# Kernel optimization log

Hardware: AMD Instinct MI355X
Metric: run time of the kernel (lower is better)

The kernel has to match this reference:

```python
import jax, jax.numpy as jnp
import numpy as np

ROPE_BASE = 10000.0

def _rope_cos_sin(T, d, dtype):
    inv_freq = 1.0 / (ROPE_BASE ** (jnp.arange(0, d, 2, dtype=jnp.float32) / d))
    t = jnp.arange(T, dtype=jnp.float32)
    freqs = t[:, None] * inv_freq[None, :]           # [T, d/2]
    emb = jnp.concatenate([freqs, freqs], axis=-1)   # [T, d]
    return jnp.cos(emb).astype(dtype), jnp.sin(emb).astype(dtype)

def _rotate_half(x):
    x1, x2 = jnp.split(x, 2, axis=-1)
    return jnp.concatenate([-x2, x1], axis=-1)

def setup_inputs() -> dict:
    key = jax.random.key(0)
    k1, k2, k3, k4 = jax.random.split(key, 4)
    B, T, C, H = 4, 4096, 1024, 64
    x = jax.random.normal(k1, (B, T, C), dtype=jnp.float32)
    s = 1.0 / np.sqrt(C)
    Wq = jax.random.normal(k2, (H, C), dtype=jnp.float32) * s
    Wk = jax.random.normal(k3, (H, C), dtype=jnp.float32) * s
    Wv = jax.random.normal(k4, (H, C), dtype=jnp.float32) * s
    return {"x": x, "Wq": Wq, "Wk": Wk, "Wv": Wv}

def reference(x, Wq, Wk, Wv):
    B, T, C = x.shape
    H = Wq.shape[0]
    q = jnp.einsum('btc,hc->bth', x, Wq)
    k = jnp.einsum('btc,hc->bth', x, Wk)
    v = jnp.einsum('btc,hc->bth', x, Wv)
    cos, sin = _rope_cos_sin(T, H, x.dtype)
    q = q * cos + _rotate_half(q) * sin
    k = k * cos + _rotate_half(k) * sin
    # NOTE: original scales by dim_model**-0.5 (C), not head_size
    wei = jnp.einsum('bth,bsh->bts', q, k) * (C ** -0.5)
    causal = jnp.tril(jnp.ones((T, T), dtype=bool))
    wei = jnp.where(causal, wei, -jnp.inf)
    wei = jax.nn.softmax(wei, axis=-1)
    # dropout p=0.0 (identity)
    out = jnp.einsum('bts,bsh->bth', wei, v)
    return out
```

## Files before the change

### kernel.cpp

```cpp
#include <hip/hip_runtime.h>
#include <hip/hip_bf16.h>
#include <math.h>

typedef __attribute__((ext_vector_type(8))) __bf16 bf16x8;
typedef __attribute__((ext_vector_type(4))) float f32x4;
typedef __attribute__((ext_vector_type(16))) float f32x16;
typedef __attribute__((ext_vector_type(4))) float float4_t;
typedef __attribute__((ext_vector_type(4))) unsigned int uint4_t;

#define NB 4
#define TSEQ 4096
#define CD 1024
#define HD 64
#define NCH 16
#define CHT 4
#define QBL 16

static __device__ __forceinline__ unsigned short f2bf(float f) {
    union { float f; unsigned u; } v; v.f = f;
    unsigned r = v.u + 0x7fffu + ((v.u >> 16) & 1u);
    return (unsigned short)(r >> 16);
}
static __device__ __forceinline__ float bf2f(unsigned short u) {
    union { unsigned int i; float f; } v; v.i = ((unsigned int)u) << 16;
    return v.f;
}
static __device__ __forceinline__ unsigned int pk2(float a, float b) {
    union { __bf16 h[2]; unsigned int u; } x;
    x.h[0] = (__bf16)a; x.h[1] = (__bf16)b;
    return x.u;
}

__global__ __launch_bounds__(256) void wcvt_kernel(const float* __restrict__ wq,
                                                   const float* __restrict__ wk,
                                                   const float* __restrict__ wv,
                                                   unsigned short* __restrict__ wb) {
    int i = blockIdx.x * 256 + threadIdx.x;
    int j = i >> 10;
    int col = i & 1023;
    int jb = j >> 4, off = j & 15;
    int sub = ((jb & 1) << 5) | ((jb & 2) << 3);
    int srcrow = (jb < 8) ? (sub + off) : ((jb - 8) * 16 + off);
    const float* src = (jb < 4) ? wq : ((jb < 8) ? wk : wv);
    wb[i] = f2bf(src[srcrow * 1024 + col]);
}

__global__ __launch_bounds__(256) void qkv_kernel(const float* __restrict__ x,
                                                  const unsigned short* __restrict__ wb,
                                                  unsigned short* __restrict__ qo,
                                                  unsigned short* __restrict__ ko,
                                                  unsigned short* __restrict__ vt) {
    __shared__ unsigned short xs[64][72];
    __shared__ unsigned short ws[96][72];
    const int tid = threadIdx.x;
    const int wave = tid >> 6, lane = tid & 63;
    const int lr = lane & 15;
    const int lk = (lane >> 4) << 3;
    const int rowg = (lane >> 4) << 2;
    const int row0 = blockIdx.x * 64;
    const int phase = blockIdx.y;

    f32x4 acc[6];
#pragma unroll
    for (int i = 0; i < 6; ++i) acc[i] = (f32x4){0.f, 0.f, 0.f, 0.f};

    const int sr = tid >> 2;
    const int sc = (tid & 3) << 4;
    const unsigned short* wbp = wb + (size_t)(96 * phase) * CD;

    for (int k0 = 0; k0 < CD; k0 += 64) {
        __syncthreads();
        {
            const float4_t* s4 =
                reinterpret_cast<const float4_t*>(x + (size_t)(row0 + sr) * CD + k0 + sc);
            float4_t f0 = s4[0], f1 = s4[1], f2 = s4[2], f3 = s4[3];
            uint4_t w0, w1;
            w0[0] = pk2(f0[0], f0[1]); w0[1] = pk2(f0[2], f0[3]);
            w0[2] = pk2(f1[0], f1[1]); w0[3] = pk2(f1[2], f1[3]);
            w1[0] = pk2(f2[0], f2[1]); w1[1] = pk2(f2[2], f2[3]);
            w1[2] = pk2(f3[0], f3[1]); w1[3] = pk2(f3[2], f3[3]);
            *reinterpret_cast<uint4_t*>(&xs[sr][sc]) = w0;
            *reinterpret_cast<uint4_t*>(&xs[sr][sc + 8]) = w1;
        }
#pragma unroll
        for (int i = 0; i < 3; ++i) {
            int u = tid + (i << 8);
            int r = u >> 3, c = (u & 7) << 3;
            *reinterpret_cast<uint4_t*>(&ws[r][c]) =
                *reinterpret_cast<const uint4_t*>(wbp + (size_t)r * CD + k0 + c);
        }
        __syncthreads();
#pragma unroll
        for (int kk = 0; kk < 2; ++kk) {
            bf16x8 a = *reinterpret_cast<const bf16x8*>(&xs[wave * 16 + lr][kk * 32 + lk]);
#pragma unroll
            for (int c = 0; c < 6; ++c) {
                bf16x8 bfr = *reinterpret_cast<const bf16x8*>(&ws[c * 16 + lr][kk * 32 + lk]);
                acc[c] = __builtin_amdgcn_mfma_f32_16x16x32_bf16(a, bfr, acc[c], 0, 0, 0);
            }
        }
    }

    const int gr0 = row0 + wave * 16 + rowg;
    const int bidx = gr0 >> 12;
    const int tb = gr0 & (TSEQ - 1);
    const float sc2 = 0.045084218764560315f;
    const float l2b = 0.4152410118609215f;
    const float invf0 = exp2f(-(float)lr * l2b);
    const float invf1 = exp2f(-(float)(lr + 16) * l2b);
#pragma unroll
    for (int r = 0; r < 4; ++r) {
        float t = (float)(tb + r);
        float s0, c0, s1, c1;
        sincosf(t * invf0, &s0, &c0);
        sincosf(t * invf1, &s1, &c1);
        size_t ro = (size_t)(gr0 + r) * HD;
        if (phase == 0) {
            float lo, hi;
            lo = acc[0][r]; hi = acc[1][r];
            qo[ro + 0 + lr]  = f2bf((lo * c0 - hi * s0) * sc2);
            qo[ro + 32 + lr] = f2bf((hi * c0 + lo * s0) * sc2);
            lo = acc[2][r]; hi = acc[3][r];
            qo[ro + 16 + lr] = f2bf((lo * c1 - hi * s1) * sc2);
            qo[ro + 48 + lr] = f2bf((hi * c1 + lo * s1) * sc2);
            lo = acc[4][r]; hi = acc[5][r];
            ko[ro + 0 + lr]  = f2bf(lo * c0 - hi * s0);
            ko[ro + 32 + lr] = f2bf(hi * c0 + lo * s0);
        } else {
            float lo = acc[0][r], hi = acc[1][r];
            ko[ro + 16 + lr] = f2bf(lo * c1 - hi * s1);
            ko[ro + 48 + lr] = f2bf(hi * c1 + lo * s1);
            size_t vbase = (size_t)bidx * HD * TSEQ + (size_t)(tb + r);
            vt[vbase + (size_t)(0 + lr) * TSEQ]  = f2bf(acc[2][r]);
            vt[vbase + (size_t)(16 + lr) * TSEQ] = f2bf(acc[3][r]);
            vt[vbase + (size_t)(32 + lr) * TSEQ] = f2bf(acc[4][r]);
            vt[vbase + (size_t)(48 + lr) * TSEQ] = f2bf(acc[5][r]);
        }
    }
}

__global__ __launch_bounds__(512, 4) void attn_partial(const unsigned short* __restrict__ q,
                                                       const unsigned short* __restrict__ k,
                                                       const unsigned short* __restrict__ vt,
                                                       unsigned short* __restrict__ po,
                                                       float* __restrict__ pm,
                                                       float* __restrict__ pl) {
    const int chunk = blockIdx.x, qb = blockIdx.y, b = blockIdx.z;
    const int ktend_blk = 4 * qb + 3;
    const int kt0 = chunk * CHT;
    if (kt0 > ktend_blk) return;
    const int ktend = min(ktend_blk, kt0 + CHT - 1);

    __shared__ unsigned short ks[64][72];
    __shared__ unsigned short vs[64][72];
    const int tid = threadIdx.x;
    const int wave = tid >> 6, lane = tid & 63;
    const int l31 = lane & 31;
    const int h = lane >> 5;
    const int h8 = h << 3;
    const int qrow0 = qb * 256 + wave * 32;
    const int qpos = qrow0 + l31;

    const unsigned short* qb_ = q + ((size_t)(b * TSEQ + qpos)) * HD + h8;
    bf16x8 qf[4];
#pragma unroll
    for (int s = 0; s < 4; ++s)
        qf[s] = *reinterpret_cast<const bf16x8*>(qb_ + 16 * s);

    f32x16 oacc[2];
#pragma unroll
    for (int dt = 0; dt < 2; ++dt)
#pragma unroll
        for (int r = 0; r < 16; ++r) oacc[dt][r] = 0.f;
    float mreg = -1.0e30f;
    float lsum = 0.f;

    const int srow = tid >> 3;
    const int scol = (tid & 7) << 3;
    const unsigned short* kbase = k + (size_t)b * TSEQ * HD;
    const unsigned short* vbase = vt + (size_t)b * HD * TSEQ;
    uint4_t kr, vr;

    auto loadtile = [&](int kt) {
        const int s0l = kt * 64;
        kr = *reinterpret_cast<const uint4_t*>(kbase + (size_t)(s0l + srow) * HD + scol);
        vr = *reinterpret_cast<const uint4_t*>(vbase + (size_t)srow * TSEQ + s0l + scol);
    };

    loadtile(kt0);

    for (int kt = kt0; kt <= ktend; ++kt) {
        const int s0 = kt * 64;
        __syncthreads();
        *reinterpret_cast<uint4_t*>(&ks[srow][scol]) = kr;
        *reinterpret_cast<uint4_t*>(&vs[srow][scol]) = vr;
        __syncthreads();
        if (kt < ktend) loadtile(kt + 1);

        if (s0 > qrow0 + 31) continue;

        f32x16 sacc[2];
#pragma unroll
        for (int blk = 0; blk < 2; ++blk)
#pragma unroll
            for (int r = 0; r < 16; ++r) sacc[blk][r] = 0.f;
        __builtin_amdgcn_s_setprio(1);
#pragma unroll
        for (int s = 0; s < 4; ++s) {
            bf16x8 ka = *reinterpret_cast<const bf16x8*>(&ks[l31][16 * s + h8]);
            bf16x8 kb2 = *reinterpret_cast<const bf16x8*>(&ks[32 + l31][16 * s + h8]);
            sacc[0] = __builtin_amdgcn_mfma_f32_32x32x16_bf16(ka, qf[s], sacc[0], 0, 0, 0);
            sacc[1] = __builtin_amdgcn_mfma_f32_32x32x16_bf16(kb2, qf[s], sacc[1], 0, 0, 0);
        }
        __builtin_amdgcn_s_setprio(0);

        if (s0 + 63 > qrow0) {
#pragma unroll
            for (int blk = 0; blk < 2; ++blk)
#pragma unroll
                for (int r = 0; r < 16; ++r) {
                    int kvpos = s0 + 32 * blk + (r & 3) + ((r >> 2) << 3) + (h << 2);
                    if (kvpos > qpos) sacc[blk][r] = -INFINITY;
                }
        }

        float tm[8];
#pragma unroll
        for (int r = 0; r < 8; ++r)
            tm[r] = fmaxf(fmaxf(sacc[0][r], sacc[0][r + 8]),
                          fmaxf(sacc[1][r], sacc[1][r + 8]));
#pragma unroll
        for (int r = 0; r < 4; ++r) tm[r] = fmaxf(tm[r], tm[r + 4]);
        float mx = fmaxf(fmaxf(tm[0], tm[1]), fmaxf(tm[2], tm[3]));
        mx = fmaxf(mx, __shfl_xor(mx, 32, 64));

        const bool newmax = !__all(mx <= mreg + 7.0f);
        if (newmax) {
            float mnew = fmaxf(mreg, mx);
            float corr = __builtin_amdgcn_exp2f(mreg - mnew);
            mreg = mnew;
            lsum *= corr;
#pragma unroll
            for (int dt = 0; dt < 2; ++dt)
#pragma unroll
                for (int r = 0; r < 16; ++r) oacc[dt][r] *= corr;
        }

        float pvv[2][16];
#pragma unroll
        for (int blk = 0; blk < 2; ++blk)
#pragma unroll
            for (int r = 0; r < 16; ++r)
                pvv[blk][r] = __builtin_amdgcn_exp2f(sacc[blk][r] - mreg);
        float ts[8];
#pragma unroll
        for (int r = 0; r < 8; ++r)
            ts[r] = (pvv[0][r] + pvv[0][r + 8]) + (pvv[1][r] + pvv[1][r + 8]);
#pragma unroll
        for (int r = 0; r < 4; ++r) ts[r] += ts[r + 4];
        float psum = (ts[0] + ts[1]) + (ts[2] + ts[3]);
        psum += __shfl_xor(psum, 32, 64);
        lsum += psum;

        unsigned int cw[2][4][2];
#pragma unroll
        for (int blk = 0; blk < 2; ++blk)
#pragma unroll
            for (int G = 0; G < 4; ++G) {
                cw[blk][G][0] = pk2(pvv[blk][4 * G], pvv[blk][4 * G + 1]);
                cw[blk][G][1] = pk2(pvv[blk][4 * G + 2], pvv[blk][4 * G + 3]);
            }

        const bool hif = (h == 1);
        __builtin_amdgcn_s_setprio(1);
#pragma unroll
        for (int s = 0; s < 4; ++s) {
            const int blk = s >> 1, base = (s & 1) << 1;
            unsigned int a0 = cw[blk][base][0],     a1 = cw[blk][base][1];
            unsigned int b0 = cw[blk][base + 1][0], b1 = cw[blk][base + 1][1];
            unsigned int s0w = hif ? a0 : b0;
            unsigned int s1w = hif ? a1 : b1;
            unsigned int r0 = __shfl_xor(s0w, 32, 64);
            unsigned int r1 = __shfl_xor(s1w, 32, 64);
            uint4_t pw;
            pw[0] = hif ? r0 : a0;
            pw[1] = hif ? r1 : a1;
            pw[2] = hif ? b0 : r0;
            pw[3] = hif ? b1 : r1;
            bf16x8 pfrag = *reinterpret_cast<const bf16x8*>(&pw);
            bf16x8 v0 = *reinterpret_cast<const bf16x8*>(&vs[l31][16 * s + h8]);
            bf16x8 v1 = *reinterpret_cast<const bf16x8*>(&vs[32 + l31][16 * s + h8]);
            oacc[0] = __builtin_amdgcn_mfma_f32_32x32x16_bf16(v0, pfrag, oacc[0], 0, 0, 0);
            oacc[1] = __builtin_amdgcn_mfma_f32_32x32x16_bf16(v1, pfrag, oacc[1], 0, 0, 0);
        }
        __builtin_amdgcn_s_setprio(0);
    }

    const int slot = (((b << 4) + qb) << 4) + chunk;
    unsigned short* pob = po + (size_t)slot * 16384;
#pragma unroll
    for (int dt = 0; dt < 2; ++dt)
#pragma unroll
        for (int r = 0; r < 16; ++r) {
            int d = 32 * dt + (r & 3) + ((r >> 2) << 3) + (h << 2);
            pob[d * 256 + wave * 32 + l31] = f2bf(oacc[dt][r]);
        }
    if (h == 0) {
        pm[slot * 256 + wave * 32 + l31] = mreg;
        pl[slot * 256 + wave * 32 + l31] = lsum;
    }
}

__global__ __launch_bounds__(256) void attn_combine(const unsigned short* __restrict__ po,
                                                    const float* __restrict__ pm,
                                                    const float* __restrict__ pl,
                                                    float* __restrict__ out) {
    __shared__ float sm[64][17];
    const int bq = blockIdx.x;
    const int dg = blockIdx.y;
    const int qt = bq & 63;
    const int b = bq >> 6;
    const int qb = qt >> 2, quarter = qt & 3;
    const int nch = qb + 1;
    const int qi = threadIdx.x & 63;
    const int jj = threadIdx.x >> 6;
    const int slotb = (((b << 4) + qb) << 4);
    const int qoff = quarter * 64 + qi;

    float pmv[NCH];
#pragma unroll
    for (int c = 0; c < NCH; ++c)
        pmv[c] = (c < nch) ? pm[(size_t)(slotb + c) * 256 + qoff] : -1.0e30f;
    float tmv[NCH];
#pragma unroll
    for (int c = 0; c < NCH; ++c) tmv[c] = pmv[c];
#pragma unroll
    for (int s = NCH / 2; s >= 1; s >>= 1)
#pragma unroll
        for (int c = 0; c < NCH / 2; ++c)
            if (c < s) tmv[c] = fmaxf(tmv[c], tmv[c + s]);
    const float M = tmv[0];

    float L = 0.f;
    float a0 = 0.f, a1 = 0.f, a2 = 0.f, a3 = 0.f;
    const int dbase = dg * 16 + jj * 4;
#pragma unroll 4
    for (int c = 0; c < nch; ++c) {
        float w = exp2f(pmv[c] - M);
        L += w * pl[(size_t)(slotb + c) * 256 + qoff];
        const unsigned short* p = po + (size_t)(slotb + c) * 16384 + dbase * 256 + qoff;
        a0 += w * bf2f(p[0]);
        a1 += w * bf2f(p[256]);
        a2 += w * bf2f(p[512]);
        a3 += w * bf2f(p[768]);
    }
    const float inv = 1.f / L;
    sm[qi][jj * 4 + 0] = a0 * inv;
    sm[qi][jj * 4 + 1] = a1 * inv;
    sm[qi][jj * 4 + 2] = a2 * inv;
    sm[qi][jj * 4 + 3] = a3 * inv;
    __syncthreads();
    const int row = threadIdx.x >> 2;
    const int c4 = (threadIdx.x & 3) << 2;
    float4_t f;
#pragma unroll
    for (int e = 0; e < 4; ++e) f[e] = sm[row][c4 + e];
    *reinterpret_cast<float4_t*>(out + (size_t)bq * 4096 + row * 64 + dg * 16 + c4) = f;
}

extern "C" void kernel_launch(void* const* d_in, const int* in_sizes, int n_in,
                              void* d_out, int out_size, void* d_ws, size_t ws_size,
                              hipStream_t stream) {
    const float* x = (const float*)d_in[0];
    const float* wq = (const float*)d_in[1];
    const float* wk = (const float*)d_in[2];
    const float* wv = (const float*)d_in[3];
    float* out = (float*)d_out;

    unsigned short* wb = (unsigned short*)d_ws;
    unsigned short* qb = wb + 3 * HD * CD;
    unsigned short* kb = qb + (size_t)NB * TSEQ * HD;
    unsigned short* vtb = kb + (size_t)NB * TSEQ * HD;
    unsigned short* pob = vtb + (size_t)NB * TSEQ * HD;
    float* pm = (float*)(pob + (size_t)1024 * 16384);
    float* pl = pm + (size_t)1024 * 256;

    wcvt_kernel<<<768, 256, 0, stream>>>(wq, wk, wv, wb);
    qkv_kernel<<<dim3(256, 2), 256, 0, stream>>>(x, wb, qb, kb, vtb);
    attn_partial<<<dim3(NCH, QBL, NB), 512, 0, stream>>>(qb, kb, vtb, pob, pm, pl);
    attn_combine<<<dim3(NB * 64, 4), 256, 0, stream>>>(pob, pm, pl, out);
}
```

Before: 66.64 us.

## Retile QKV projection to read x once and halve attention split-K chunks

The QKV projection now loads each 32-row tile of x once and computes all 192 output columns in one block, with waves split across rows and column halves. Before, two phase blocks each re-read and re-converted the same 64 rows of x. The attention split-K factor drops from 16 chunks of 4 key tiles to 8 chunks of 8, which halves the partial-output storage and the combine traffic. The trade-off is longer serial work per attention block and fewer blocks, which can hurt load balance on the causal triangle.

```diff
diff --git a/kernel.cpp b/kernel.cpp
--- a/kernel.cpp
+++ b/kernel.cpp
@@ -12,8 +12,8 @@
 #define TSEQ 4096
 #define CD 1024
 #define HD 64
-#define NCH 16
-#define CHT 4
+#define NCH 8
+#define CHT 8
 #define QBL 16
 
 static __device__ __forceinline__ unsigned short f2bf(float f) {
@@ -50,58 +50,55 @@
                                                   unsigned short* __restrict__ qo,
                                                   unsigned short* __restrict__ ko,
                                                   unsigned short* __restrict__ vt) {
-    __shared__ unsigned short xs[64][72];
-    __shared__ unsigned short ws[96][72];
+    __shared__ unsigned short xs[32][72];
+    __shared__ unsigned short ws[192][72];
     const int tid = threadIdx.x;
     const int wave = tid >> 6, lane = tid & 63;
     const int lr = lane & 15;
     const int lk = (lane >> 4) << 3;
     const int rowg = (lane >> 4) << 2;
-    const int row0 = blockIdx.x * 64;
-    const int phase = blockIdx.y;
+    const int wr = wave & 1, wc = wave >> 1;
+    const int row0 = blockIdx.x * 32;
 
     f32x4 acc[6];
 #pragma unroll
     for (int i = 0; i < 6; ++i) acc[i] = (f32x4){0.f, 0.f, 0.f, 0.f};
 
-    const int sr = tid >> 2;
-    const int sc = (tid & 3) << 4;
-    const unsigned short* wbp = wb + (size_t)(96 * phase) * CD;
+    const int xr = tid >> 3;
+    const int xc = (tid & 7) << 3;
 
     for (int k0 = 0; k0 < CD; k0 += 64) {
         __syncthreads();
         {
             const float4_t* s4 =
-                reinterpret_cast<const float4_t*>(x + (size_t)(row0 + sr) * CD + k0 + sc);
-            float4_t f0 = s4[0], f1 = s4[1], f2 = s4[2], f3 = s4[3];
-            uint4_t w0, w1;
+                reinterpret_cast<const float4_t*>(x + (size_t)(row0 + xr) * CD + k0 + xc);
+            float4_t f0 = s4[0], f1 = s4[1];
+            uint4_t w0;
             w0[0] = pk2(f0[0], f0[1]); w0[1] = pk2(f0[2], f0[3]);
             w0[2] = pk2(f1[0], f1[1]); w0[3] = pk2(f1[2], f1[3]);
-            w1[0] = pk2(f2[0], f2[1]); w1[1] = pk2(f2[2], f2[3]);
-            w1[2] = pk2(f3[0], f3[1]); w1[3] = pk2(f3[2], f3[3]);
-            *reinterpret_cast<uint4_t*>(&xs[sr][sc]) = w0;
-            *reinterpret_cast<uint4_t*>(&xs[sr][sc + 8]) = w1;
-        }
-#pragma unroll
-        for (int i = 0; i < 3; ++i) {
+            *reinterpret_cast<uint4_t*>(&xs[xr][xc]) = w0;
+        }
+#pragma unroll
+        for (int i = 0; i < 6; ++i) {
             int u = tid + (i << 8);
-            int r = u >> 3, c = (u & 7) << 3;
-            *reinterpret_cast<uint4_t*>(&ws[r][c]) =
-                *reinterpret_cast<const uint4_t*>(wbp + (size_t)r * CD + k0 + c);
+            int r = u >> 3, c8 = (u & 7) << 3;
+            *reinterpret_cast<uint4_t*>(&ws[r][c8]) =
+                *reinterpret_cast<const uint4_t*>(wb + (size_t)r * CD + k0 + c8);
         }
         __syncthreads();
 #pragma unroll
         for (int kk = 0; kk < 2; ++kk) {
-            bf16x8 a = *reinterpret_cast<const bf16x8*>(&xs[wave * 16 + lr][kk * 32 + lk]);
+            bf16x8 a = *reinterpret_cast<const bf16x8*>(&xs[wr * 16 + lr][kk * 32 + lk]);
 #pragma unroll
             for (int c = 0; c < 6; ++c) {
-                bf16x8 bfr = *reinterpret_cast<const bf16x8*>(&ws[c * 16 + lr][kk * 32 + lk]);
+                bf16x8 bfr =
+                    *reinterpret_cast<const bf16x8*>(&ws[wc * 96 + c * 16 + lr][kk * 32 + lk]);
                 acc[c] = __builtin_amdgcn_mfma_f32_16x16x32_bf16(a, bfr, acc[c], 0, 0, 0);
             }
         }
     }
 
-    const int gr0 = row0 + wave * 16 + rowg;
+    const int gr0 = row0 + wr * 16 + rowg;
     const int bidx = gr0 >> 12;
     const int tb = gr0 & (TSEQ - 1);
     const float sc2 = 0.045084218764560315f;
@@ -115,7 +112,7 @@
         sincosf(t * invf0, &s0, &c0);
         sincosf(t * invf1, &s1, &c1);
         size_t ro = (size_t)(gr0 + r) * HD;
-        if (phase == 0) {
+        if (wc == 0) {
             float lo, hi;
             lo = acc[0][r]; hi = acc[1][r];
             qo[ro + 0 + lr]  = f2bf((lo * c0 - hi * s0) * sc2);
@@ -296,7 +293,7 @@
         __builtin_amdgcn_s_setprio(0);
     }
 
-    const int slot = (((b << 4) + qb) << 4) + chunk;
+    const int slot = (((b << 4) + qb) << 3) + chunk;
     unsigned short* pob = po + (size_t)slot * 16384;
 #pragma unroll
     for (int dt = 0; dt < 2; ++dt)
@@ -321,10 +318,10 @@
     const int qt = bq & 63;
     const int b = bq >> 6;
     const int qb = qt >> 2, quarter = qt & 3;
-    const int nch = qb + 1;
+    const int nch = (4 * qb + 11) >> 3;
     const int qi = threadIdx.x & 63;
     const int jj = threadIdx.x >> 6;
-    const int slotb = (((b << 4) + qb) << 4);
+    const int slotb = (((b << 4) + qb) << 3);
     const int qoff = quarter * 64 + qi;
 
     float pmv[NCH];
@@ -382,11 +379,11 @@
     unsigned short* kb = qb + (size_t)NB * TSEQ * HD;
     unsigned short* vtb = kb + (size_t)NB * TSEQ * HD;
     unsigned short* pob = vtb + (size_t)NB * TSEQ * HD;
-    float* pm = (float*)(pob + (size_t)1024 * 16384);
-    float* pl = pm + (size_t)1024 * 256;
+    float* pm = (float*)(pob + (size_t)512 * 16384);
+    float* pl = pm + (size_t)512 * 256;
 
     wcvt_kernel<<<768, 256, 0, stream>>>(wq, wk, wv, wb);
-    qkv_kernel<<<dim3(256, 2), 256, 0, stream>>>(x, wb, qb, kb, vtb);
+    qkv_kernel<<<512, 256, 0, stream>>>(x, wb, qb, kb, vtb);
     attn_partial<<<dim3(NCH, QBL, NB), 512, 0, stream>>>(qb, kb, vtb, pob, pm, pl);
     attn_combine<<<dim3(NB * 64, 4), 256, 0, stream>>>(pob, pm, pl, out);
 }
```

After: 64.31 us. 1.04x faster.
